# Optimization experiments

Measured on AMD Instinct MI355X. Metric: run time of the kernel, lower is better.

Reference implementation:

```python
import jax, jax.numpy as jnp
import numpy as np

DIM = 2048
HID = 5632
ZERO_POINT = 128.0


def _qlinear(x, wq, scale):
    # wq: uint8-style codes stored as int32, shape [out, in]; scale: [out]
    W = (wq.astype(jnp.float32) - ZERO_POINT) * scale[:, None]  # dequant [out, in]
    return jnp.einsum('bsd,hd->bsh', x, W)


def setup_inputs() -> dict:
    key = jax.random.key(0)
    ks = jax.random.split(key, 7)
    B, S = 4, 2048
    # scale chosen so dequantized weights have ~1/sqrt(fan_in) magnitude
    sg = jax.random.uniform(ks[1], (HID,)) * (0.02 / np.sqrt(DIM)) + 1e-4
    su = jax.random.uniform(ks[3], (HID,)) * (0.02 / np.sqrt(DIM)) + 1e-4
    sd = jax.random.uniform(ks[5], (DIM,)) * (0.02 / np.sqrt(HID)) + 1e-4
    return {
        'x': jax.random.normal(ks[0], (B, S, DIM), dtype=jnp.float32),
        'wq_gate': jax.random.randint(ks[2], (HID, DIM), 0, 256, dtype=jnp.int32),
        's_gate': sg,
        'wq_up': jax.random.randint(ks[4], (HID, DIM), 0, 256, dtype=jnp.int32),
        's_up': su,
        'wq_down': jax.random.randint(ks[6], (DIM, HID), 0, 256, dtype=jnp.int32),
        's_down': sd,
    }


def reference(x, wq_gate, s_gate, wq_up, s_up, wq_down, s_down):
    gate = _qlinear(x, wq_gate, s_gate)          # [B, S, HID]
    gate = jax.nn.silu(gate)
    up = _qlinear(x, wq_up, s_up)                # [B, S, HID]
    return _qlinear(gate * up, wq_down, s_down)  # [B, S, DIM]
```

## Files before the change

### kernel.cpp

```cpp
#include <hip/hip_runtime.h>
#include <hip/hip_bf16.h>
#include <stdint.h>

#define DIM 2048
#define HID 5632

typedef __attribute__((ext_vector_type(8))) short short8;
typedef __attribute__((ext_vector_type(4))) float f32x4;
typedef __attribute__((ext_vector_type(4))) int int4v;
typedef __attribute__((ext_vector_type(4))) unsigned short ushort4v;

__device__ __forceinline__ unsigned short f32_to_bf16_rne(float f) {
    union { float f; unsigned u; } v; v.f = f;
    unsigned u = v.u;
    return (unsigned short)((u + 0x7FFFu + ((u >> 16) & 1u)) >> 16);
}

__device__ __forceinline__ void gload16(const void* g, void* l) {
    __builtin_amdgcn_global_load_lds(
        (const __attribute__((address_space(1))) void*)g,
        (__attribute__((address_space(3))) void*)l,
        16, 0, 0);
}

__global__ void dequant_plain(const int* __restrict__ wq, const float* __restrict__ scale,
                              unsigned short* __restrict__ out, long total, int cols) {
    long n4 = total >> 2;
    long stride = (long)gridDim.x * blockDim.x;
    for (long i = (long)blockIdx.x * blockDim.x + threadIdx.x; i < n4; i += stride) {
        int4v c = ((const int4v*)wq)[i];
        int row = (int)((i << 2) / cols);
        float s = scale[row];
        ushort4v o;
        o.x = f32_to_bf16_rne(((float)c.x - 128.0f) * s);
        o.y = f32_to_bf16_rne(((float)c.y - 128.0f) * s);
        o.z = f32_to_bf16_rne(((float)c.z - 128.0f) * s);
        o.w = f32_to_bf16_rne(((float)c.w - 128.0f) * s);
        ((ushort4v*)out)[i] = o;
    }
}

__global__ void dequant_gateup(const int* __restrict__ wg, const float* __restrict__ sg,
                               const int* __restrict__ wu, const float* __restrict__ su,
                               unsigned short* __restrict__ out) {
    const long n4 = (long)HID * DIM / 4;
    long stride = (long)gridDim.x * blockDim.x;
    for (long i = (long)blockIdx.x * blockDim.x + threadIdx.x; i < n4; i += stride) {
        int r  = (int)(i >> 9);
        int c4 = (int)(i & 511);
        int rp = ((r >> 4) << 5) + (r & 15);
        float s1 = sg[r], s2 = su[r];
        int4v g = ((const int4v*)wg)[i];
        int4v u = ((const int4v*)wu)[i];
        ushort4v og, ou;
        og.x = f32_to_bf16_rne(((float)g.x - 128.0f) * s1);
        og.y = f32_to_bf16_rne(((float)g.y - 128.0f) * s1);
        og.z = f32_to_bf16_rne(((float)g.z - 128.0f) * s1);
        og.w = f32_to_bf16_rne(((float)g.w - 128.0f) * s1);
        ou.x = f32_to_bf16_rne(((float)u.x - 128.0f) * s2);
        ou.y = f32_to_bf16_rne(((float)u.y - 128.0f) * s2);
        ou.z = f32_to_bf16_rne(((float)u.z - 128.0f) * s2);
        ou.w = f32_to_bf16_rne(((float)u.w - 128.0f) * s2);
        ((ushort4v*)out)[(long)rp * 512 + c4]        = og;
        ((ushort4v*)out)[(long)(rp + 16) * 512 + c4] = ou;
    }
}

__global__ void cast_f32_bf16(const float* __restrict__ in, unsigned short* __restrict__ out, long n) {
    long n4 = n >> 2;
    long stride = (long)gridDim.x * blockDim.x;
    for (long i = (long)blockIdx.x * blockDim.x + threadIdx.x; i < n4; i += stride) {
        f32x4 v = ((const f32x4*)in)[i];
        ushort4v o;
        o.x = f32_to_bf16_rne(v[0]);
        o.y = f32_to_bf16_rne(v[1]);
        o.z = f32_to_bf16_rne(v[2]);
        o.w = f32_to_bf16_rne(v[3]);
        ((ushort4v*)out)[i] = o;
    }
}


__global__ __launch_bounds__(512, 2) void gemm_gateup(
    const unsigned short* __restrict__ X,
    const unsigned short* __restrict__ Wp,
    unsigned short* __restrict__ H)
{
    __shared__ __attribute__((aligned(16))) unsigned short As[2][256 * 64];
    __shared__ __attribute__((aligned(16))) unsigned short Bs[2][256 * 64];

    const int q  = (int)(gridDim.x >> 3);
    const int wg = (blockIdx.x & 7) * q + (blockIdx.x >> 3);
    const int bx = wg & 31;
    const int by = wg >> 5;

    const int tid  = threadIdx.x;
    const int lane = tid & 63;
    const int wid  = tid >> 6;
    const int wr   = wid >> 2;
    const int wc   = wid & 3;
    const int m0   = bx << 8;
    const int n0   = by << 8;
    const int lr   = lane & 15;
    const int kg   = lane >> 4;

    int srow[4], skc[4], sdst[4];
    #pragma unroll
    for (int l = 0; l < 4; ++l) {
        int p = l * 512 + tid;
        srow[l] = p >> 3;
        skc[l]  = (((p & 7) ^ ((p >> 3) & 7)) << 3);
        sdst[l] = p << 3;
    }

    auto STAGE = [&](int buf, int kt) {
        const int kk = kt << 6;
        #pragma unroll
        for (int l = 0; l < 4; ++l) {
            gload16(X  + (size_t)(m0 + srow[l]) * DIM + kk + skc[l], &As[buf][sdst[l]]);
            gload16(Wp + (size_t)(n0 + srow[l]) * DIM + kk + skc[l], &Bs[buf][sdst[l]]);
        }
    };

    f32x4 acc[8][4];
    #pragma unroll
    for (int m = 0; m < 8; ++m)
        #pragma unroll
        for (int n = 0; n < 4; ++n) acc[m][n] = (f32x4){0.f, 0.f, 0.f, 0.f};

    const int c0 = ((kg ^ (lr & 7)) << 3);
    const int c1 = (((4 + kg) ^ (lr & 7)) << 3);
    const int abase = (wr * 128 + lr) * 64;
    const int bbase = (wc * 64 + lr) * 64;

    STAGE(0, 0);
    STAGE(1, 1);

    const int NT = DIM / 64;
    for (int kt = 0; kt < NT; ++kt) {
        const int cur = kt & 1;
        if (kt < NT - 1) asm volatile("s_waitcnt vmcnt(8)" ::: "memory");
        else             asm volatile("s_waitcnt vmcnt(0)" ::: "memory");
        __builtin_amdgcn_s_barrier();
        __builtin_amdgcn_sched_barrier(0);

        const unsigned short* ap0 = &As[cur][abase + c0];
        const unsigned short* ap1 = &As[cur][abase + c1];
        const unsigned short* bp0 = &Bs[cur][bbase + c0];
        const unsigned short* bp1 = &Bs[cur][bbase + c1];

        short8 a0[8], a1[8], b0[4], b1[4];
        #pragma unroll
        for (int n = 0; n < 4; ++n) {
            b0[n] = *(const short8*)(bp0 + (n << 10));
            b1[n] = *(const short8*)(bp1 + (n << 10));
        }
        #pragma unroll
        for (int m = 0; m < 8; ++m) {
            a0[m] = *(const short8*)(ap0 + (m << 10));
            a1[m] = *(const short8*)(ap1 + (m << 10));
        }

        __builtin_amdgcn_s_setprio(1);
        #pragma unroll
        for (int m = 0; m < 8; ++m)
            #pragma unroll
            for (int n = 0; n < 4; ++n)
                acc[m][n] = __builtin_amdgcn_mfma_f32_16x16x32_bf16(a0[m], b0[n], acc[m][n], 0, 0, 0);
        __builtin_amdgcn_s_setprio(0);
        __builtin_amdgcn_s_setprio(1);
        #pragma unroll
        for (int m = 0; m < 8; ++m)
            #pragma unroll
            for (int n = 0; n < 4; ++n)
                acc[m][n] = __builtin_amdgcn_mfma_f32_16x16x32_bf16(a1[m], b1[n], acc[m][n], 0, 0, 0);
        __builtin_amdgcn_s_setprio(0);

        __builtin_amdgcn_sched_barrier(0);
        __builtin_amdgcn_s_barrier();
        __builtin_amdgcn_sched_barrier(0);
        if (kt + 2 < NT) STAGE(cur, kt + 2);
        __builtin_amdgcn_sched_barrier(0);
    }

    const int lg = lane >> 4;
    #pragma unroll
    for (int m = 0; m < 8; ++m) {
        #pragma unroll
        for (int i = 0; i < 2; ++i) {
            f32x4 g = acc[m][2 * i], u = acc[m][2 * i + 1];
            const int col = (by << 7) + wc * 32 + i * 16 + lr;
            #pragma unroll
            for (int e = 0; e < 4; ++e) {
                const int row = m0 + wr * 128 + m * 16 + lg * 4 + e;
                float gv = g[e];
                float sg = gv / (1.0f + __expf(-gv));
                H[(size_t)row * HID + col] = f32_to_bf16_rne(sg * u[e]);
            }
        }
    }
}

__global__ __launch_bounds__(512, 2) void gemm_down(
    const unsigned short* __restrict__ Hb,
    const unsigned short* __restrict__ Wd,
    float* __restrict__ Out)
{
    __shared__ __attribute__((aligned(16))) unsigned short As[2][256 * 64];
    __shared__ __attribute__((aligned(16))) unsigned short Bs[2][256 * 64];

    const int q  = (int)(gridDim.x >> 3);
    const int wg = (blockIdx.x & 7) * q + (blockIdx.x >> 3);
    const int bx = wg & 31;
    const int by = wg >> 5;

    const int tid  = threadIdx.x;
    const int lane = tid & 63;
    const int wid  = tid >> 6;
    const int wr   = wid >> 2;
    const int wc   = wid & 3;
    const int m0   = bx << 8;
    const int n0   = by << 8;
    const int lr   = lane & 15;
    const int kg   = lane >> 4;

    int srow[4], skc[4], sdst[4];
    #pragma unroll
    for (int l = 0; l < 4; ++l) {
        int p = l * 512 + tid;
        srow[l] = p >> 3;
        skc[l]  = (((p & 7) ^ ((p >> 3) & 7)) << 3);
        sdst[l] = p << 3;
    }

    auto STAGE = [&](int buf, int kt) {
        const int kk = kt << 6;
        #pragma unroll
        for (int l = 0; l < 4; ++l) {
            gload16(Hb + (size_t)(m0 + srow[l]) * HID + kk + skc[l], &As[buf][sdst[l]]);
            gload16(Wd + (size_t)(n0 + srow[l]) * HID + kk + skc[l], &Bs[buf][sdst[l]]);
        }
    };

    f32x4 acc[8][4];
    #pragma unroll
    for (int m = 0; m < 8; ++m)
        #pragma unroll
        for (int n = 0; n < 4; ++n) acc[m][n] = (f32x4){0.f, 0.f, 0.f, 0.f};

    const int c0 = ((kg ^ (lr & 7)) << 3);
    const int c1 = (((4 + kg) ^ (lr & 7)) << 3);
    const int abase = (wr * 128 + lr) * 64;
    const int bbase = (wc * 64 + lr) * 64;

    STAGE(0, 0);
    STAGE(1, 1);

    const int NT = HID / 64;
    for (int kt = 0; kt < NT; ++kt) {
        const int cur = kt & 1;
        if (kt < NT - 1) asm volatile("s_waitcnt vmcnt(8)" ::: "memory");
        else             asm volatile("s_waitcnt vmcnt(0)" ::: "memory");
        __builtin_amdgcn_s_barrier();
        __builtin_amdgcn_sched_barrier(0);

        const unsigned short* ap0 = &As[cur][abase + c0];
        const unsigned short* ap1 = &As[cur][abase + c1];
        const unsigned short* bp0 = &Bs[cur][bbase + c0];
        const unsigned short* bp1 = &Bs[cur][bbase + c1];

        short8 a0[8], a1[8], b0[4], b1[4];
        #pragma unroll
        for (int n = 0; n < 4; ++n) {
            b0[n] = *(const short8*)(bp0 + (n << 10));
            b1[n] = *(const short8*)(bp1 + (n << 10));
        }
        #pragma unroll
        for (int m = 0; m < 8; ++m) {
            a0[m] = *(const short8*)(ap0 + (m << 10));
            a1[m] = *(const short8*)(ap1 + (m << 10));
        }

        __builtin_amdgcn_s_setprio(1);
        #pragma unroll
        for (int m = 0; m < 8; ++m)
            #pragma unroll
            for (int n = 0; n < 4; ++n)
                acc[m][n] = __builtin_amdgcn_mfma_f32_16x16x32_bf16(a0[m], b0[n], acc[m][n], 0, 0, 0);
        __builtin_amdgcn_s_setprio(0);
        __builtin_amdgcn_s_setprio(1);
        #pragma unroll
        for (int m = 0; m < 8; ++m)
            #pragma unroll
            for (int n = 0; n < 4; ++n)
                acc[m][n] = __builtin_amdgcn_mfma_f32_16x16x32_bf16(a1[m], b1[n], acc[m][n], 0, 0, 0);
        __builtin_amdgcn_s_setprio(0);

        __builtin_amdgcn_sched_barrier(0);
        __builtin_amdgcn_s_barrier();
        __builtin_amdgcn_sched_barrier(0);
        if (kt + 2 < NT) STAGE(cur, kt + 2);
        __builtin_amdgcn_sched_barrier(0);
    }

    const int lg = lane >> 4;
    #pragma unroll
    for (int m = 0; m < 8; ++m) {
        #pragma unroll
        for (int n = 0; n < 4; ++n) {
            const int col = n0 + wc * 64 + n * 16 + lr;
            #pragma unroll
            for (int e = 0; e < 4; ++e) {
                const int row = m0 + wr * 128 + m * 16 + lg * 4 + e;
                Out[(size_t)row * DIM + col] = acc[m][n][e];
            }
        }
    }
}

extern "C" void kernel_launch(void* const* d_in, const int* in_sizes, int n_in,
                              void* d_out, int out_size, void* d_ws, size_t ws_size,
                              hipStream_t stream) {
    const float* x      = (const float*)d_in[0];
    const int* wq_gate  = (const int*)d_in[1];
    const float* s_gate = (const float*)d_in[2];
    const int* wq_up    = (const int*)d_in[3];
    const float* s_up   = (const float*)d_in[4];
    const int* wq_down  = (const int*)d_in[5];
    const float* s_down = (const float*)d_in[6];
    float* out = (float*)d_out;

    const int M = in_sizes[0] / DIM;

    unsigned short* xb  = (unsigned short*)d_ws;
    unsigned short* wgu = xb + (size_t)M * DIM;
    unsigned short* h   = wgu + (size_t)2 * HID * DIM;

    cast_f32_bf16<<<2048, 256, 0, stream>>>(x, xb, (long)M * DIM);
    dequant_gateup<<<2048, 256, 0, stream>>>(wq_gate, s_gate, wq_up, s_up, wgu);

    gemm_gateup<<<(M / 256) * ((2 * HID) / 256), 512, 0, stream>>>(xb, wgu, h);

    dequant_plain<<<2048, 256, 0, stream>>>(wq_down, s_down, wgu, (long)DIM * HID, HID);

    gemm_down<<<(M / 256) * (DIM / 256), 512, 0, stream>>>(h, wgu, out);
}
```

Baseline: 608.8 us.

## Make gate/up GEMM persistent over N tiles and drop XCD block swizzle

The gate/up GEMM becomes a persistent kernel with 256 workgroups. Each workgroup owns one M row block and walks 5 or 6 N tiles with stride 8. It prefetches the next tile's first two K stages while it runs the SiLU·up epilogue of the current tile, which hides the pipeline fill and drain between tiles. The XCD-aware block index remap is removed from both GEMMs, and the down GEMM now uses a 2D grid. The loop body is factored into a macro. The risk is worse L2 locality across XCDs and load imbalance between workgroups with 5 and 6 tiles, and the code hard-codes M=8192 (32 row blocks, 30+2 K-steps).

```diff
diff --git a/kernel.cpp b/kernel.cpp
--- a/kernel.cpp
+++ b/kernel.cpp
@@ -80,6 +80,44 @@
     }
 }
 
+#define KSTEP(CURBUF, VMN)                                                            \
+    asm volatile("s_waitcnt vmcnt(" #VMN ")" ::: "memory");                           \
+    __builtin_amdgcn_s_barrier();                                                     \
+    __builtin_amdgcn_sched_barrier(0);                                                \
+    {                                                                                 \
+        const unsigned short* ap0 = &As[CURBUF][abase + c0];                          \
+        const unsigned short* ap1 = &As[CURBUF][abase + c1];                          \
+        const unsigned short* bp0 = &Bs[CURBUF][bbase + c0];                          \
+        const unsigned short* bp1 = &Bs[CURBUF][bbase + c1];                          \
+        short8 a0[8], a1[8], b0[4], b1[4];                                            \
+        _Pragma("unroll")                                                             \
+        for (int n = 0; n < 4; ++n) {                                                 \
+            b0[n] = *(const short8*)(bp0 + (n << 10));                                \
+            b1[n] = *(const short8*)(bp1 + (n << 10));                                \
+        }                                                                             \
+        _Pragma("unroll")                                                             \
+        for (int m = 0; m < 8; ++m) {                                                 \
+            a0[m] = *(const short8*)(ap0 + (m << 10));                                \
+            a1[m] = *(const short8*)(ap1 + (m << 10));                                \
+        }                                                                             \
+        __builtin_amdgcn_s_setprio(1);                                                \
+        _Pragma("unroll")                                                             \
+        for (int m = 0; m < 8; ++m)                                                   \
+            _Pragma("unroll")                                                         \
+            for (int n = 0; n < 4; ++n)                                               \
+                acc[m][n] = __builtin_amdgcn_mfma_f32_16x16x32_bf16(a0[m], b0[n], acc[m][n], 0, 0, 0); \
+        __builtin_amdgcn_s_setprio(0);                                                \
+        __builtin_amdgcn_s_setprio(1);                                                \
+        _Pragma("unroll")                                                             \
+        for (int m = 0; m < 8; ++m)                                                   \
+            _Pragma("unroll")                                                         \
+            for (int n = 0; n < 4; ++n)                                               \
+                acc[m][n] = __builtin_amdgcn_mfma_f32_16x16x32_bf16(a1[m], b1[n], acc[m][n], 0, 0, 0); \
+        __builtin_amdgcn_s_setprio(0);                                                \
+    }                                                                                 \
+    __builtin_amdgcn_sched_barrier(0);                                                \
+    __builtin_amdgcn_s_barrier();                                                     \
+    __builtin_amdgcn_sched_barrier(0);
 
 __global__ __launch_bounds__(512, 2) void gemm_gateup(
     const unsigned short* __restrict__ X,
@@ -89,18 +127,17 @@
     __shared__ __attribute__((aligned(16))) unsigned short As[2][256 * 64];
     __shared__ __attribute__((aligned(16))) unsigned short Bs[2][256 * 64];
 
-    const int q  = (int)(gridDim.x >> 3);
-    const int wg = (blockIdx.x & 7) * q + (blockIdx.x >> 3);
-    const int bx = wg & 31;
-    const int by = wg >> 5;
+    const int bid    = blockIdx.x;
+    const int bx     = bid & 31;
+    const int byBase = bid >> 5;
+    const int ntiles = (byBase < 4) ? 6 : 5;
+    const int m0     = bx << 8;
 
     const int tid  = threadIdx.x;
     const int lane = tid & 63;
     const int wid  = tid >> 6;
     const int wr   = wid >> 2;
     const int wc   = wid & 3;
-    const int m0   = bx << 8;
-    const int n0   = by << 8;
     const int lr   = lane & 15;
     const int kg   = lane >> 4;
 
@@ -113,12 +150,12 @@
         sdst[l] = p << 3;
     }
 
-    auto STAGE = [&](int buf, int kt) {
+    auto STAGE = [&](int n0v, int kt, int buf) {
         const int kk = kt << 6;
         #pragma unroll
         for (int l = 0; l < 4; ++l) {
-            gload16(X  + (size_t)(m0 + srow[l]) * DIM + kk + skc[l], &As[buf][sdst[l]]);
-            gload16(Wp + (size_t)(n0 + srow[l]) * DIM + kk + skc[l], &Bs[buf][sdst[l]]);
+            gload16(X  + (size_t)(m0  + srow[l]) * DIM + kk + skc[l], &As[buf][sdst[l]]);
+            gload16(Wp + (size_t)(n0v + srow[l]) * DIM + kk + skc[l], &Bs[buf][sdst[l]]);
         }
     };
 
@@ -132,72 +169,55 @@
     const int c1 = (((4 + kg) ^ (lr & 7)) << 3);
     const int abase = (wr * 128 + lr) * 64;
     const int bbase = (wc * 64 + lr) * 64;
-
-    STAGE(0, 0);
-    STAGE(1, 1);
-
-    const int NT = DIM / 64;
-    for (int kt = 0; kt < NT; ++kt) {
-        const int cur = kt & 1;
-        if (kt < NT - 1) asm volatile("s_waitcnt vmcnt(8)" ::: "memory");
-        else             asm volatile("s_waitcnt vmcnt(0)" ::: "memory");
-        __builtin_amdgcn_s_barrier();
+    const int lg = lane >> 4;
+
+    {
+        const int n00 = byBase << 8;
+        STAGE(n00, 0, 0);
+        STAGE(n00, 1, 1);
+    }
+
+    for (int j = 0; j < ntiles; ++j) {
+        const int by   = byBase + (j << 3);
+        const int n0   = by << 8;
+        const int n0n  = n0 + (8 << 8);
+        const bool hasNext = (j + 1 < ntiles);
+
+        #pragma unroll 2
+        for (int kt = 0; kt < 30; ++kt) {
+            const int cur = kt & 1;
+            KSTEP(cur, 8)
+            STAGE(n0, kt + 2, cur);
+            __builtin_amdgcn_sched_barrier(0);
+        }
+        KSTEP(0, 8)
+        if (hasNext) STAGE(n0n, 0, 0);
         __builtin_amdgcn_sched_barrier(0);
-
-        const unsigned short* ap0 = &As[cur][abase + c0];
-        const unsigned short* ap1 = &As[cur][abase + c1];
-        const unsigned short* bp0 = &Bs[cur][bbase + c0];
-        const unsigned short* bp1 = &Bs[cur][bbase + c1];
-
-        short8 a0[8], a1[8], b0[4], b1[4];
-        #pragma unroll
-        for (int n = 0; n < 4; ++n) {
-            b0[n] = *(const short8*)(bp0 + (n << 10));
-            b1[n] = *(const short8*)(bp1 + (n << 10));
-        }
+        if (hasNext) { KSTEP(1, 8) }
+        else         { KSTEP(1, 0) }
+
         #pragma unroll
         for (int m = 0; m < 8; ++m) {
-            a0[m] = *(const short8*)(ap0 + (m << 10));
-            a1[m] = *(const short8*)(ap1 + (m << 10));
-        }
-
-        __builtin_amdgcn_s_setprio(1);
+            #pragma unroll
+            for (int i = 0; i < 2; ++i) {
+                f32x4 g = acc[m][2 * i], u = acc[m][2 * i + 1];
+                const int col = (by << 7) + wc * 32 + i * 16 + lr;
+                #pragma unroll
+                for (int e = 0; e < 4; ++e) {
+                    const int row = m0 + wr * 128 + m * 16 + lg * 4 + e;
+                    float gv = g[e];
+                    float sg = gv / (1.0f + __expf(-gv));
+                    H[(size_t)row * HID + col] = f32_to_bf16_rne(sg * u[e]);
+                }
+            }
+        }
         #pragma unroll
         for (int m = 0; m < 8; ++m)
             #pragma unroll
-            for (int n = 0; n < 4; ++n)
-                acc[m][n] = __builtin_amdgcn_mfma_f32_16x16x32_bf16(a0[m], b0[n], acc[m][n], 0, 0, 0);
-        __builtin_amdgcn_s_setprio(0);
-        __builtin_amdgcn_s_setprio(1);
-        #pragma unroll
-        for (int m = 0; m < 8; ++m)
-            #pragma unroll
-            for (int n = 0; n < 4; ++n)
-                acc[m][n] = __builtin_amdgcn_mfma_f32_16x16x32_bf16(a1[m], b1[n], acc[m][n], 0, 0, 0);
-        __builtin_amdgcn_s_setprio(0);
-
+            for (int n = 0; n < 4; ++n) acc[m][n] = (f32x4){0.f, 0.f, 0.f, 0.f};
+
+        if (hasNext) STAGE(n0n, 1, 1);
         __builtin_amdgcn_sched_barrier(0);
-        __builtin_amdgcn_s_barrier();
-        __builtin_amdgcn_sched_barrier(0);
-        if (kt + 2 < NT) STAGE(cur, kt + 2);
-        __builtin_amdgcn_sched_barrier(0);
-    }
-
-    const int lg = lane >> 4;
-    #pragma unroll
-    for (int m = 0; m < 8; ++m) {
-        #pragma unroll
-        for (int i = 0; i < 2; ++i) {
-            f32x4 g = acc[m][2 * i], u = acc[m][2 * i + 1];
-            const int col = (by << 7) + wc * 32 + i * 16 + lr;
-            #pragma unroll
-            for (int e = 0; e < 4; ++e) {
-                const int row = m0 + wr * 128 + m * 16 + lg * 4 + e;
-                float gv = g[e];
-                float sg = gv / (1.0f + __expf(-gv));
-                H[(size_t)row * HID + col] = f32_to_bf16_rne(sg * u[e]);
-            }
-        }
     }
 }
 
@@ -209,18 +229,13 @@
     __shared__ __attribute__((aligned(16))) unsigned short As[2][256 * 64];
     __shared__ __attribute__((aligned(16))) unsigned short Bs[2][256 * 64];
 
-    const int q  = (int)(gridDim.x >> 3);
-    const int wg = (blockIdx.x & 7) * q + (blockIdx.x >> 3);
-    const int bx = wg & 31;
-    const int by = wg >> 5;
-
     const int tid  = threadIdx.x;
     const int lane = tid & 63;
     const int wid  = tid >> 6;
     const int wr   = wid >> 2;
     const int wc   = wid & 3;
-    const int m0   = bx << 8;
-    const int n0   = by << 8;
+    const int m0   = blockIdx.x << 8;
+    const int n0   = blockIdx.y << 8;
     const int lr   = lane & 15;
     const int kg   = lane >> 4;
 
@@ -259,46 +274,8 @@
     const int NT = HID / 64;
     for (int kt = 0; kt < NT; ++kt) {
         const int cur = kt & 1;
-        if (kt < NT - 1) asm volatile("s_waitcnt vmcnt(8)" ::: "memory");
-        else             asm volatile("s_waitcnt vmcnt(0)" ::: "memory");
-        __builtin_amdgcn_s_barrier();
-        __builtin_amdgcn_sched_barrier(0);
-
-        const unsigned short* ap0 = &As[cur][abase + c0];
-        const unsigned short* ap1 = &As[cur][abase + c1];
-        const unsigned short* bp0 = &Bs[cur][bbase + c0];
-        const unsigned short* bp1 = &Bs[cur][bbase + c1];
-
-        short8 a0[8], a1[8], b0[4], b1[4];
-        #pragma unroll
-        for (int n = 0; n < 4; ++n) {
-            b0[n] = *(const short8*)(bp0 + (n << 10));
-            b1[n] = *(const short8*)(bp1 + (n << 10));
-        }
-        #pragma unroll
-        for (int m = 0; m < 8; ++m) {
-            a0[m] = *(const short8*)(ap0 + (m << 10));
-            a1[m] = *(const short8*)(ap1 + (m << 10));
-        }
-
-        __builtin_amdgcn_s_setprio(1);
-        #pragma unroll
-        for (int m = 0; m < 8; ++m)
-            #pragma unroll
-            for (int n = 0; n < 4; ++n)
-                acc[m][n] = __builtin_amdgcn_mfma_f32_16x16x32_bf16(a0[m], b0[n], acc[m][n], 0, 0, 0);
-        __builtin_amdgcn_s_setprio(0);
-        __builtin_amdgcn_s_setprio(1);
-        #pragma unroll
-        for (int m = 0; m < 8; ++m)
-            #pragma unroll
-            for (int n = 0; n < 4; ++n)
-                acc[m][n] = __builtin_amdgcn_mfma_f32_16x16x32_bf16(a1[m], b1[n], acc[m][n], 0, 0, 0);
-        __builtin_amdgcn_s_setprio(0);
-
-        __builtin_amdgcn_sched_barrier(0);
-        __builtin_amdgcn_s_barrier();
-        __builtin_amdgcn_sched_barrier(0);
+        if (kt < NT - 1) { KSTEP(cur, 8) }
+        else             { KSTEP(cur, 0) }
         if (kt + 2 < NT) STAGE(cur, kt + 2);
         __builtin_amdgcn_sched_barrier(0);
     }
@@ -339,9 +316,9 @@
     cast_f32_bf16<<<2048, 256, 0, stream>>>(x, xb, (long)M * DIM);
     dequant_gateup<<<2048, 256, 0, stream>>>(wq_gate, s_gate, wq_up, s_up, wgu);
 
-    gemm_gateup<<<(M / 256) * ((2 * HID) / 256), 512, 0, stream>>>(xb, wgu, h);
+    gemm_gateup<<<256, 512, 0, stream>>>(xb, wgu, h);
 
     dequant_plain<<<2048, 256, 0, stream>>>(wq_down, s_down, wgu, (long)DIM * HID, HID);
 
-    gemm_down<<<(M / 256) * (DIM / 256), 512, 0, stream>>>(h, wgu, out);
-}
+    gemm_down<<<dim3(M / 256, DIM / 256), 512, 0, stream>>>(h, wgu, out);
+}
```

Measured after the change: 967.0 us. 58.8% more time.
